# Optimization experiments

Hardware: AMD Instinct MI355X
Metric: run time of the kernel (lower is better)

Reference implementation:

```python
import jax, jax.numpy as jnp
import numpy as np

N, D, C, T = 8192, 64, 100, 30  # samples, embedding_dim, n_classes, n_transforms (initialize_radial_flow n_transforms=30)
LOG_EV_CLAMP = 10.0             # EvidenceScaler clamp on log evidence
EV_BUDGET = 0.5 * D * float(np.log(4.0 * np.pi))  # 'normal' evidence budget: 0.5*dim*log(4*pi)


def setup_inputs() -> dict:
    key = jax.random.key(0)
    ks = jax.random.split(key, 8)
    x = jax.random.normal(ks[0], (N, D), dtype=jnp.float32)          # embeddings (base = identity here)
    labels = jax.random.randint(ks[1], (N,), 0, C)                   # int class labels
    freq = jax.random.uniform(ks[2], (C,), dtype=jnp.float32) + 0.1
    freq = freq / freq.sum()                                         # labels_frequency (sums to 1)
    # per-class radial flow params: z0 [C,T,D], alpha' [C,T], beta' [C,T]
    z0 = jax.random.normal(ks[3], (C, T, D), dtype=jnp.float32) * 0.1
    alpha_prime = jax.random.normal(ks[4], (C, T), dtype=jnp.float32) * 0.1
    beta_prime = jax.random.normal(ks[5], (C, T), dtype=jnp.float32) * 0.1
    W = jax.random.normal(ks[6], (D, C), dtype=jnp.float32) / np.sqrt(D)  # CategoricalOutput linear
    b = jnp.zeros((C,), jnp.float32)
    return dict(x=x, labels=labels, labels_frequency=freq, z0=z0,
                alpha_prime=alpha_prime, beta_prime=beta_prime, W=W, b=b)


def _flow_log_prob(x, z0s, aps, bps):
    """Radial normalizing flow log-density (density direction): log N(f(x)) + log|det df/dx|.
    x: [N, D]; z0s: [T, D]; aps, bps: [T]."""
    def step(carry, params):
        z, ld = carry
        z0, ap, bp = params
        alpha = jax.nn.softplus(ap)
        beta = -alpha + jax.nn.softplus(bp)   # beta > -alpha ensures invertibility
        diff = z - z0                          # [N, D]
        r = jnp.linalg.norm(diff, axis=-1)     # [N]
        h = 1.0 / (alpha + r)
        bh = beta * h
        z_new = z + bh[:, None] * diff
        # log|det| = (D-1)*log(1+beta*h) + log(1 + beta*h + beta*h'*r), h' = -h^2
        ld_new = ld + (D - 1) * jnp.log1p(bh) + jnp.log1p(bh * (1.0 - h * r))
        return (z_new, ld_new), None

    init = (x, jnp.zeros(x.shape[0], x.dtype))
    (z, ld), _ = jax.lax.scan(step, init, (z0s, aps, bps))
    base = -0.5 * (D * jnp.log(2.0 * jnp.pi) + jnp.sum(z * z, axis=-1))  # standard normal base
    return base + ld


def reference(x, labels, labels_frequency, z0, alpha_prime, beta_prime, W, b):
    # per-class flow log-probs for ALL samples: [C, N] (dispatch-compute, vectorized over classes)
    lp = jax.vmap(_flow_log_prob, in_axes=(None, 0, 0, 0))(x, z0, alpha_prime, beta_prime)
    # class_specific_log_prob: gather each sample's own-class log-prob (the boolean-mask gather/scatter loop)
    class_lp = jnp.take_along_axis(lp, labels[None, :], axis=0)[0]            # [N]
    # marginalize_log_prob: logsumexp over classes with log class frequencies
    marg = jax.nn.logsumexp(lp + jnp.log(labels_frequency)[:, None], axis=0)  # [N]
    # EvidenceScaler('normal') + clamp, then NatPN Dirichlet posterior update
    log_ev = jnp.minimum(marg + EV_BUDGET, LOG_EV_CLAMP)                      # [N]
    probs = jax.nn.softmax(x @ W + b, axis=-1)                                # expected sufficient statistics
    alpha = 1.0 + jnp.exp(log_ev)[:, None] * probs                            # prior alpha=1 + evidence*stats
    # output: [N, C+1] = [log alpha | class-specific log-prob]
    return jnp.concatenate([jnp.log(alpha), class_lp[:, None]], axis=1)
```

## Files before the change

### kernel.cpp

```cpp
#include <hip/hip_runtime.h>
#include <math.h>

#define N 8192
#define D 64
#define C 100
#define T 30
#define GSTRIDE 32
#define ZROWS 32
#define CROWS 112
#define WSTRIDE 20
#define SB 16

static constexpr float D_LOG_2PI      = 117.62413225019811f;
static constexpr float EV_BUDGET_F    = 80.992775903017304f;
static constexpr float LOG_EV_CLAMP_F = 10.0f;

typedef __attribute__((ext_vector_type(8))) short short8x;
typedef __attribute__((ext_vector_type(4))) float floatx4;

static __device__ __forceinline__ unsigned short f2bf(float f) {
    __bf16 h = (__bf16)f;
    return __builtin_bit_cast(unsigned short, h);
}

#define AS_CONST __attribute__((address_space(4)))
typedef const AS_CONST floatx4* cfp4_t;
static __device__ __forceinline__ floatx4 sload4(const float* p) {
    return *(cfp4_t)(unsigned long long)p;
}

__global__ __launch_bounds__(256) void megaprep_kernel(
        const float* __restrict__ x,
        const float* __restrict__ z0,
        const float* __restrict__ ap,
        const float* __restrict__ bp,
        const float* __restrict__ W,
        unsigned short* __restrict__ xbf,
        float* __restrict__ q0,
        float* __restrict__ Gp,
        float* __restrict__ abgt,
        unsigned short* __restrict__ z0bf,
        unsigned short* __restrict__ wtbf) {
    const int blk = blockIdx.x;

    if (blk < 256) {
        const int r = blk * 32 + (threadIdx.x >> 3);
        const int e = threadIdx.x & 7;
        const float4* xp = (const float4*)(x + (size_t)r * D + e * 8);
        const float4 a = xp[0], b = xp[1];
        short8x o;
        o[0] = f2bf(a.x); o[1] = f2bf(a.y); o[2] = f2bf(a.z); o[3] = f2bf(a.w);
        o[4] = f2bf(b.x); o[5] = f2bf(b.y); o[6] = f2bf(b.z); o[7] = f2bf(b.w);
        *(short8x*)(xbf + (size_t)r * D + e * 8) = o;
        float q = a.x*a.x + a.y*a.y + a.z*a.z + a.w*a.w
                + b.x*b.x + b.y*b.y + b.z*b.z + b.w*b.w;
        q += __shfl_xor(q, 4, 8);
        q += __shfl_xor(q, 2, 8);
        q += __shfl_xor(q, 1, 8);
        if (e == 0) q0[r] = q;
        return;
    }

    if (blk >= 356) {
        const int i = (blk - 356) * 256 + threadIdx.x;
        const int c = i >> 6, d = i & 63;
        wtbf[i] = f2bf(c < C ? W[d * C + c] : 0.0f);
        return;
    }

    const int c = blk - 256;
    __shared__ float z0s[T * D];
    for (int i = threadIdx.x; i < T * D; i += blockDim.x)
        z0s[i] = z0[c * T * D + i];
    __syncthreads();

    for (int idx = threadIdx.x; idx < T * GSTRIDE; idx += blockDim.x) {
        const int u = idx >> 5, v = idx & 31;
        float s = 0.0f;
        if (v < T) {
            #pragma unroll
            for (int d = 0; d < D; ++d)
                s = fmaf(z0s[u * D + d], z0s[v * D + d], s);
        }
        Gp[(size_t)c * T * GSTRIDE + idx] = s;
    }

    for (int i = threadIdx.x; i < ZROWS * D; i += blockDim.x) {
        const int u = i >> 6;
        z0bf[(size_t)c * ZROWS * D + i] = f2bf(u < T ? z0s[u * D + (i & 63)] : 0.0f);
    }

    if (threadIdx.x < T) {
        const int t = threadIdx.x;
        const float a = ap[c * T + t];
        const float b = bp[c * T + t];
        const float spa = fmaxf(a, 0.0f) + log1pf(expf(-fabsf(a)));
        const float spb = fmaxf(b, 0.0f) + log1pf(expf(-fabsf(b)));
        float gtt = 0.0f;
        #pragma unroll
        for (int d = 0; d < D; ++d)
            gtt = fmaf(z0s[t * D + d], z0s[t * D + d], gtt);
        float* o = abgt + ((size_t)c * T + t) * 4;
        o[0] = spa;
        o[1] = -spa + spb;
        o[2] = gtt;
        o[3] = 0.0f;
    }
}

__global__ __launch_bounds__(256, 2) void flow_kernel(
        const unsigned short* __restrict__ xbf,
        const float* __restrict__ q0g,
        const unsigned short* __restrict__ z0bf,
        const float* __restrict__ Gp,
        const float* __restrict__ abgt,
        float* __restrict__ lp) {
    const int c    = blockIdx.y;
    const int wv   = threadIdx.x >> 6;
    const int ln   = threadIdx.x & 63;
    const int col  = ln & 15;
    const int quad = ln >> 4;
    const int nb   = blockIdx.x * 512 + wv * 128;

    __shared__ float wlds[4][64 * WSTRIDE];

    const unsigned short* zb = z0bf + (size_t)c * ZROWS * D;
    short8x A[2][2];
    #pragma unroll
    for (int mu = 0; mu < 2; ++mu) {
        A[mu][0] = *(const short8x*)(zb + (mu * 16 + col) * D + quad * 8);
        A[mu][1] = *(const short8x*)(zb + (mu * 16 + col) * D + 32 + quad * 8);
    }

    float w[2][ZROWS];
    #pragma unroll
    for (int half = 0; half < 2; ++half) {
        const int hb = nb + half * 64;
        #pragma unroll
        for (int mu = 0; mu < 2; ++mu) {
            floatx4 acc[4];
            #pragma unroll
            for (int nt = 0; nt < 4; ++nt) acc[nt] = (floatx4)(0.0f);
            #pragma unroll
            for (int nt = 0; nt < 4; ++nt) {
                const unsigned short* bp_ =
                    xbf + (size_t)(hb + nt * 16 + col) * D + quad * 8;
                const short8x B0 = *(const short8x*)(bp_);
                acc[nt] = __builtin_amdgcn_mfma_f32_16x16x32_bf16(A[mu][0], B0, acc[nt], 0, 0, 0);
                const short8x B1 = *(const short8x*)(bp_ + 32);
                acc[nt] = __builtin_amdgcn_mfma_f32_16x16x32_bf16(A[mu][1], B1, acc[nt], 0, 0, 0);
            }
            #pragma unroll
            for (int nt = 0; nt < 4; ++nt)
                *(floatx4*)&wlds[wv][(nt * 16 + col) * WSTRIDE + quad * 4] = acc[nt];
            #pragma unroll
            for (int j = 0; j < 4; ++j) {
                const float4 t = *(const float4*)&wlds[wv][ln * WSTRIDE + j * 4];
                w[half][mu * 16 + 4 * j + 0] = t.x;
                w[half][mu * 16 + 4 * j + 1] = t.y;
                w[half][mu * 16 + 4 * j + 2] = t.z;
                w[half][mu * 16 + 4 * j + 3] = t.w;
            }
        }
    }

    const float* gb = Gp + (size_t)c * T * GSTRIDE;
    const float* ab = abgt + ((size_t)c * T) * 4;

    float qA = q0g[nb + ln], qB = q0g[nb + 64 + ln];
    float PA = 1.0f, PB = 1.0f;
    float pfA = 1.0f, pfB = 1.0f;
    float pgA = 1.0f, pgB = 1.0f;
    #pragma unroll
    for (int t = 0; t < T; ++t) {
        const floatx4 av = sload4(ab + t * 4);
        const float alpha = av[0], beta = av[1], Gtt = av[2];

        const float wtA = PA * w[0][t];
        float r2A = fmaf(-2.0f, wtA, qA) + Gtt;
        r2A = fmaxf(r2A, 0.0f);
        const float rA  = __builtin_amdgcn_sqrtf(r2A);
        const float hA  = __builtin_amdgcn_rcpf(alpha + rA);
        const float bhA = beta * hA;
        const float fA  = 1.0f + bhA;
        pfA *= fA;
        pgA *= fmaf(bhA * alpha, hA, 1.0f);
        float qnA = fA * fA * qA;
        qnA = fmaf(bhA * fA, -2.0f * wtA, qnA);
        qnA = fmaf(bhA * bhA, Gtt, qnA);
        qA = qnA;
        const float PnA = PA * fA;
        const float kA  = bhA * __builtin_amdgcn_rcpf(PnA);
        PA = PnA;

        const float wtB = PB * w[1][t];
        float r2B = fmaf(-2.0f, wtB, qB) + Gtt;
        r2B = fmaxf(r2B, 0.0f);
        const float rB  = __builtin_amdgcn_sqrtf(r2B);
        const float hB  = __builtin_amdgcn_rcpf(alpha + rB);
        const float bhB = beta * hB;
        const float fB  = 1.0f + bhB;
        pfB *= fB;
        pgB *= fmaf(bhB * alpha, hB, 1.0f);
        float qnB = fB * fB * qB;
        qnB = fmaf(bhB * fB, -2.0f * wtB, qnB);
        qnB = fmaf(bhB * bhB, Gtt, qnB);
        qB = qnB;
        const float PnB = PB * fB;
        const float kB  = bhB * __builtin_amdgcn_rcpf(PnB);
        PB = PnB;

        #pragma unroll
        for (int m4 = 0; m4 < 8; ++m4) {
            if (m4 < (t >> 2)) continue;
            const floatx4 g = sload4(gb + t * GSTRIDE + 4 * m4);
            w[0][4 * m4 + 0] = fmaf(-kA, g[0], w[0][4 * m4 + 0]);
            w[0][4 * m4 + 1] = fmaf(-kA, g[1], w[0][4 * m4 + 1]);
            w[0][4 * m4 + 2] = fmaf(-kA, g[2], w[0][4 * m4 + 2]);
            w[0][4 * m4 + 3] = fmaf(-kA, g[3], w[0][4 * m4 + 3]);
            w[1][4 * m4 + 0] = fmaf(-kB, g[0], w[1][4 * m4 + 0]);
            w[1][4 * m4 + 1] = fmaf(-kB, g[1], w[1][4 * m4 + 1]);
            w[1][4 * m4 + 2] = fmaf(-kB, g[2], w[1][4 * m4 + 2]);
            w[1][4 * m4 + 3] = fmaf(-kB, g[3], w[1][4 * m4 + 3]);
        }
    }
    const float ldA = 63.0f * __logf(pfA) + __logf(pgA);
    const float ldB = 63.0f * __logf(pfB) + __logf(pgB);

    lp[(size_t)c * N + nb + ln]      = -0.5f * (D_LOG_2PI + qA) + ldA;
    lp[(size_t)c * N + nb + 64 + ln] = -0.5f * (D_LOG_2PI + qB) + ldB;
}

__global__ __launch_bounds__(256) void epilogue_kernel(
        const float* __restrict__ lp,
        const unsigned short* __restrict__ xbf,
        const unsigned short* __restrict__ wtbf,
        const float* __restrict__ b,
        const int* __restrict__ labels,
        const float* __restrict__ freq,
        float* __restrict__ out) {
    const int n0  = blockIdx.x * SB;
    const int tid = threadIdx.x;
    const int wv  = tid >> 6;
    const int ln  = tid & 63;

    __shared__ float lps[SB][101];
    __shared__ float lgs[SB][CROWS];
    __shared__ float lf[C];
    __shared__ float bsm[C];
    __shared__ int   lbl[SB];

    if (wv == 0) {
        const int col  = ln & 15;
        const int quad = ln >> 4;
        const unsigned short* bp_ = xbf + (size_t)(n0 + col) * D + quad * 8;
        const short8x B0 = *(const short8x*)(bp_);
        const short8x B1 = *(const short8x*)(bp_ + 32);
        #pragma unroll
        for (int ct = 0; ct < 7; ++ct) {
            const unsigned short* apq = wtbf + (size_t)(ct * 16 + col) * D + quad * 8;
            const short8x A0 = *(const short8x*)(apq);
            const short8x A1 = *(const short8x*)(apq + 32);
            floatx4 acc = (floatx4)(0.0f);
            acc = __builtin_amdgcn_mfma_f32_16x16x32_bf16(A0, B0, acc, 0, 0, 0);
            acc = __builtin_amdgcn_mfma_f32_16x16x32_bf16(A1, B1, acc, 0, 0, 0);
            #pragma unroll
            for (int j = 0; j < 4; ++j)
                lgs[col][ct * 16 + quad * 4 + j] = acc[j];
        }
    } else {
        for (int i = tid - 64; i < C * SB; i += 192) {
            const int cc = i >> 4, s = i & (SB - 1);
            lps[s][cc] = lp[(size_t)cc * N + n0 + s];
        }
        if (tid - 64 < C) {
            const int t2 = tid - 64;
            lf[t2]  = __logf(freq[t2]);
            bsm[t2] = b[t2];
        }
        if (tid >= 192 && tid < 192 + SB)
            lbl[tid - 192] = labels[n0 + (tid - 192)];
    }
    __syncthreads();

    const int s = tid >> 4;
    const int k = tid & 15;
    const int n = n0 + s;

    float lgt[7];
    float lm = -INFINITY;
    float vm = -INFINITY, vs = 0.0f;
    #pragma unroll
    for (int j = 0; j < 7; ++j) {
        const int cc = k + 16 * j;
        if (cc < C) {
            const float v = lps[s][cc] + lf[cc];
            const float m2 = fmaxf(vm, v);
            vs = vs * __expf(vm - m2) + __expf(v - m2);
            vm = m2;
            lgt[j] = lgs[s][cc] + bsm[cc];
            lm = fmaxf(lm, lgt[j]);
        } else lgt[j] = -INFINITY;
    }

    #pragma unroll
    for (int off = 8; off >= 1; off >>= 1) {
        const float om = __shfl_xor(vm, off, 16);
        const float os = __shfl_xor(vs, off, 16);
        const float m2 = fmaxf(vm, om);
        vs = vs * __expf(vm - m2) + os * __expf(om - m2);
        vm = m2;
        lm = fmaxf(lm, __shfl_xor(lm, off, 16));
    }
    const float marg = vm + __logf(vs);
    const float ev = __expf(fminf(marg + EV_BUDGET_F, LOG_EV_CLAMP_F));

    float ls = 0.0f;
    #pragma unroll
    for (int j = 0; j < 7; ++j)
        if (k + 16 * j < C) ls += __expf(lgt[j] - lm);
    #pragma unroll
    for (int off = 8; off >= 1; off >>= 1)
        ls += __shfl_xor(ls, off, 16);

    const float inv = ev / ls;
    float* __restrict__ outr = out + (size_t)n * (C + 1);
    #pragma unroll
    for (int j = 0; j < 7; ++j) {
        const int cc = k + 16 * j;
        if (cc < C) outr[cc] = log1pf(__expf(lgt[j] - lm) * inv);
    }
    if (k == 0) outr[C] = lps[s][lbl[s]];
}

extern "C" void kernel_launch(void* const* d_in, const int* in_sizes, int n_in,
                              void* d_out, int out_size, void* d_ws, size_t ws_size,
                              hipStream_t stream) {
    const float* x      = (const float*)d_in[0];
    const int*   labels = (const int*)  d_in[1];
    const float* freq   = (const float*)d_in[2];
    const float* z0     = (const float*)d_in[3];
    const float* ap     = (const float*)d_in[4];
    const float* bp     = (const float*)d_in[5];
    const float* W      = (const float*)d_in[6];
    const float* b      = (const float*)d_in[7];
    float* out = (float*)d_out;

    float* ws     = (float*)d_ws;
    float* lp     = ws;
    float* Gp     = lp + (size_t)C * N;
    float* abgt   = Gp + (size_t)C * T * GSTRIDE;
    unsigned short* z0bf = (unsigned short*)(abgt + (size_t)C * T * 4);
    unsigned short* xbf  = z0bf + (size_t)C * ZROWS * D;
    unsigned short* wtbf = xbf + (size_t)N * D;
    float* q0     = (float*)(wtbf + (size_t)CROWS * D);

    megaprep_kernel<<<384, 256, 0, stream>>>(x, z0, ap, bp, W,
                                             xbf, q0, Gp, abgt, z0bf, wtbf);
    flow_kernel<<<dim3(N / 512, C), 256, 0, stream>>>(xbf, q0, z0bf, Gp, abgt, lp);
    epilogue_kernel<<<N / SB, 256, 0, stream>>>(lp, xbf, wtbf, b, labels, freq, out);
}
```

Baseline: 141.5 us.

## Pack flow recurrence into float2 ops with single-wave blocks and cache prefetch

Rewrites the per-sample flow recurrence so the two samples each lane owns are kept in float2 vectors, letting the compiler emit packed FMA/mul instructions (v_pk_fma_f32) for the w updates and q recurrences. The flow kernel is relaunched as 64-thread single-wave blocks over 128 samples each, with a smaller LDS buffer. Each wave also touches the per-class G and alpha/beta tables up front to warm the cache. Packed math roughly halves VALU issue for the dominant update loop, at the cost of more blocks and extra prefetch loads.

Measured after the change: 153.2 us. 1.08x slower.

```diff
diff --git a/kernel.cpp b/kernel.cpp
--- a/kernel.cpp
+++ b/kernel.cpp
@@ -17,6 +17,7 @@
 
 typedef __attribute__((ext_vector_type(8))) short short8x;
 typedef __attribute__((ext_vector_type(4))) float floatx4;
+typedef __attribute__((ext_vector_type(2))) float floatx2;
 
 static __device__ __forceinline__ unsigned short f2bf(float f) {
     __bf16 h = (__bf16)f;
@@ -27,6 +28,13 @@
 typedef const AS_CONST floatx4* cfp4_t;
 static __device__ __forceinline__ floatx4 sload4(const float* p) {
     return *(cfp4_t)(unsigned long long)p;
+}
+
+static __device__ __forceinline__ floatx2 sp(float s) {
+    floatx2 v; v.x = s; v.y = s; return v;
+}
+static __device__ __forceinline__ floatx2 fma2(floatx2 a, floatx2 b, floatx2 c) {
+    return __builtin_elementwise_fma(a, b, c);
 }
 
 __global__ __launch_bounds__(256) void megaprep_kernel(
@@ -108,7 +116,7 @@
     }
 }
 
-__global__ __launch_bounds__(256, 2) void flow_kernel(
+__global__ __launch_bounds__(64, 4) void flow_kernel(
         const unsigned short* __restrict__ xbf,
         const float* __restrict__ q0g,
         const unsigned short* __restrict__ z0bf,
@@ -116,13 +124,26 @@
         const float* __restrict__ abgt,
         float* __restrict__ lp) {
     const int c    = blockIdx.y;
-    const int wv   = threadIdx.x >> 6;
-    const int ln   = threadIdx.x & 63;
+    const int ln   = threadIdx.x;
     const int col  = ln & 15;
     const int quad = ln >> 4;
-    const int nb   = blockIdx.x * 512 + wv * 128;
-
-    __shared__ float wlds[4][64 * WSTRIDE];
+    const int nb   = blockIdx.x * 128;
+
+    __shared__ float wlds[64 * WSTRIDE];
+
+    const float* gb = Gp + (size_t)c * T * GSTRIDE;
+    const float* ab = abgt + ((size_t)c * T) * 4;
+
+    {
+        const float4* gpre = (const float4*)gb;
+        const float4 d0 = gpre[ln];
+        const float4 d1 = gpre[ln + 64];
+        const float4 d2 = gpre[ln + 128];
+        const float4 d3 = gpre[ln + 176];
+        const float4* apre = (const float4*)ab;
+        const float4 d4 = apre[ln < 30 ? ln : 29];
+        asm volatile("" :: "v"(d0.x), "v"(d1.x), "v"(d2.x), "v"(d3.x), "v"(d4.x));
+    }
 
     const unsigned short* zb = z0bf + (size_t)c * ZROWS * D;
     short8x A[2][2];
@@ -132,7 +153,7 @@
         A[mu][1] = *(const short8x*)(zb + (mu * 16 + col) * D + 32 + quad * 8);
     }
 
-    float w[2][ZROWS];
+    floatx2 w2[ZROWS];
     #pragma unroll
     for (int half = 0; half < 2; ++half) {
         const int hb = nb + half * 64;
@@ -152,83 +173,78 @@
             }
             #pragma unroll
             for (int nt = 0; nt < 4; ++nt)
-                *(floatx4*)&wlds[wv][(nt * 16 + col) * WSTRIDE + quad * 4] = acc[nt];
+                *(floatx4*)&wlds[(nt * 16 + col) * WSTRIDE + quad * 4] = acc[nt];
             #pragma unroll
             for (int j = 0; j < 4; ++j) {
-                const float4 t = *(const float4*)&wlds[wv][ln * WSTRIDE + j * 4];
-                w[half][mu * 16 + 4 * j + 0] = t.x;
-                w[half][mu * 16 + 4 * j + 1] = t.y;
-                w[half][mu * 16 + 4 * j + 2] = t.z;
-                w[half][mu * 16 + 4 * j + 3] = t.w;
+                const float4 t = *(const float4*)&wlds[ln * WSTRIDE + j * 4];
+                if (half == 0) {
+                    w2[mu * 16 + 4 * j + 0].x = t.x;
+                    w2[mu * 16 + 4 * j + 1].x = t.y;
+                    w2[mu * 16 + 4 * j + 2].x = t.z;
+                    w2[mu * 16 + 4 * j + 3].x = t.w;
+                } else {
+                    w2[mu * 16 + 4 * j + 0].y = t.x;
+                    w2[mu * 16 + 4 * j + 1].y = t.y;
+                    w2[mu * 16 + 4 * j + 2].y = t.z;
+                    w2[mu * 16 + 4 * j + 3].y = t.w;
+                }
             }
         }
     }
 
-    const float* gb = Gp + (size_t)c * T * GSTRIDE;
-    const float* ab = abgt + ((size_t)c * T) * 4;
-
-    float qA = q0g[nb + ln], qB = q0g[nb + 64 + ln];
-    float PA = 1.0f, PB = 1.0f;
-    float pfA = 1.0f, pfB = 1.0f;
-    float pgA = 1.0f, pgB = 1.0f;
+    floatx2 q2;
+    q2.x = q0g[nb + ln];
+    q2.y = q0g[nb + 64 + ln];
+    floatx2 P2  = sp(1.0f);
+    floatx2 pf2 = sp(1.0f);
+    floatx2 pg2 = sp(1.0f);
     #pragma unroll
     for (int t = 0; t < T; ++t) {
         const floatx4 av = sload4(ab + t * 4);
         const float alpha = av[0], beta = av[1], Gtt = av[2];
 
-        const float wtA = PA * w[0][t];
-        float r2A = fmaf(-2.0f, wtA, qA) + Gtt;
-        r2A = fmaxf(r2A, 0.0f);
-        const float rA  = __builtin_amdgcn_sqrtf(r2A);
-        const float hA  = __builtin_amdgcn_rcpf(alpha + rA);
-        const float bhA = beta * hA;
-        const float fA  = 1.0f + bhA;
-        pfA *= fA;
-        pgA *= fmaf(bhA * alpha, hA, 1.0f);
-        float qnA = fA * fA * qA;
-        qnA = fmaf(bhA * fA, -2.0f * wtA, qnA);
-        qnA = fmaf(bhA * bhA, Gtt, qnA);
-        qA = qnA;
-        const float PnA = PA * fA;
-        const float kA  = bhA * __builtin_amdgcn_rcpf(PnA);
-        PA = PnA;
-
-        const float wtB = PB * w[1][t];
-        float r2B = fmaf(-2.0f, wtB, qB) + Gtt;
-        r2B = fmaxf(r2B, 0.0f);
-        const float rB  = __builtin_amdgcn_sqrtf(r2B);
-        const float hB  = __builtin_amdgcn_rcpf(alpha + rB);
-        const float bhB = beta * hB;
-        const float fB  = 1.0f + bhB;
-        pfB *= fB;
-        pgB *= fmaf(bhB * alpha, hB, 1.0f);
-        float qnB = fB * fB * qB;
-        qnB = fmaf(bhB * fB, -2.0f * wtB, qnB);
-        qnB = fmaf(bhB * bhB, Gtt, qnB);
-        qB = qnB;
-        const float PnB = PB * fB;
-        const float kB  = bhB * __builtin_amdgcn_rcpf(PnB);
-        PB = PnB;
+        const floatx2 wt2 = P2 * w2[t];
+        const floatx2 nw2 = sp(-2.0f) * wt2;
+        floatx2 r2v = (q2 + nw2) + sp(Gtt);
+        r2v.x = fmaxf(r2v.x, 0.0f);
+        r2v.y = fmaxf(r2v.y, 0.0f);
+        floatx2 r_;
+        r_.x = __builtin_amdgcn_sqrtf(r2v.x);
+        r_.y = __builtin_amdgcn_sqrtf(r2v.y);
+        const floatx2 ar = r_ + sp(alpha);
+        floatx2 h2;
+        h2.x = __builtin_amdgcn_rcpf(ar.x);
+        h2.y = __builtin_amdgcn_rcpf(ar.y);
+        const floatx2 bh2 = sp(beta) * h2;
+        const floatx2 f2v = sp(1.0f) + bh2;
+        pf2 *= f2v;
+        pg2 *= fma2(bh2 * sp(alpha), h2, sp(1.0f));
+        floatx2 qn2 = (f2v * f2v) * q2;
+        qn2 = fma2(bh2 * f2v, nw2, qn2);
+        qn2 = fma2(bh2 * bh2, sp(Gtt), qn2);
+        q2 = qn2;
+        const floatx2 Pn2 = P2 * f2v;
+        floatx2 ip2;
+        ip2.x = __builtin_amdgcn_rcpf(Pn2.x);
+        ip2.y = __builtin_amdgcn_rcpf(Pn2.y);
+        const floatx2 nk2 = -(bh2 * ip2);
+        P2 = Pn2;
 
         #pragma unroll
         for (int m4 = 0; m4 < 8; ++m4) {
             if (m4 < (t >> 2)) continue;
             const floatx4 g = sload4(gb + t * GSTRIDE + 4 * m4);
-            w[0][4 * m4 + 0] = fmaf(-kA, g[0], w[0][4 * m4 + 0]);
-            w[0][4 * m4 + 1] = fmaf(-kA, g[1], w[0][4 * m4 + 1]);
-            w[0][4 * m4 + 2] = fmaf(-kA, g[2], w[0][4 * m4 + 2]);
-            w[0][4 * m4 + 3] = fmaf(-kA, g[3], w[0][4 * m4 + 3]);
-            w[1][4 * m4 + 0] = fmaf(-kB, g[0], w[1][4 * m4 + 0]);
-            w[1][4 * m4 + 1] = fmaf(-kB, g[1], w[1][4 * m4 + 1]);
-            w[1][4 * m4 + 2] = fmaf(-kB, g[2], w[1][4 * m4 + 2]);
-            w[1][4 * m4 + 3] = fmaf(-kB, g[3], w[1][4 * m4 + 3]);
-        }
-    }
-    const float ldA = 63.0f * __logf(pfA) + __logf(pgA);
-    const float ldB = 63.0f * __logf(pfB) + __logf(pgB);
-
-    lp[(size_t)c * N + nb + ln]      = -0.5f * (D_LOG_2PI + qA) + ldA;
-    lp[(size_t)c * N + nb + 64 + ln] = -0.5f * (D_LOG_2PI + qB) + ldB;
+            w2[4 * m4 + 0] = fma2(nk2, sp(g[0]), w2[4 * m4 + 0]);
+            w2[4 * m4 + 1] = fma2(nk2, sp(g[1]), w2[4 * m4 + 1]);
+            w2[4 * m4 + 2] = fma2(nk2, sp(g[2]), w2[4 * m4 + 2]);
+            w2[4 * m4 + 3] = fma2(nk2, sp(g[3]), w2[4 * m4 + 3]);
+        }
+    }
+    const float ldA = 63.0f * __logf(pf2.x) + __logf(pg2.x);
+    const float ldB = 63.0f * __logf(pf2.y) + __logf(pg2.y);
+
+    lp[(size_t)c * N + nb + ln]      = -0.5f * (D_LOG_2PI + q2.x) + ldA;
+    lp[(size_t)c * N + nb + 64 + ln] = -0.5f * (D_LOG_2PI + q2.y) + ldB;
 }
 
 __global__ __launch_bounds__(256) void epilogue_kernel(
@@ -357,6 +373,6 @@
 
     megaprep_kernel<<<384, 256, 0, stream>>>(x, z0, ap, bp, W,
                                              xbf, q0, Gp, abgt, z0bf, wtbf);
-    flow_kernel<<<dim3(N / 512, C), 256, 0, stream>>>(xbf, q0, z0bf, Gp, abgt, lp);
+    flow_kernel<<<dim3(N / 128, C), 64, 0, stream>>>(xbf, q0, z0bf, Gp, abgt, lp);
     epilogue_kernel<<<N / SB, 256, 0, stream>>>(lp, xbf, wtbf, b, labels, freq, out);
 }
```

## Process four sample groups per lane in flow kernel and prefetch flow params

Applied to the files above, without the earlier changes.

Each thread now carries four 64-sample groups through the 30-step radial flow recurrence instead of two, which halves the grid along N. The per-step scalar parameter loads and G-matrix loads are amortized over twice as many samples, and the four independent chains expose more instruction-level parallelism. A dummy prefetch of the per-class G and alpha/beta tables is added at kernel start to warm the cache. The change roughly doubles register pressure for the w arrays (4x32 floats) under launch_bounds(256,2), which risks spills or lower occupancy, and gives fewer blocks (800 vs 1600) to fill the GPU.

Result: faster. 135.0 us (-4.5%).

```diff
diff --git a/kernel.cpp b/kernel.cpp
--- a/kernel.cpp
+++ b/kernel.cpp
@@ -120,9 +120,22 @@
     const int ln   = threadIdx.x & 63;
     const int col  = ln & 15;
     const int quad = ln >> 4;
-    const int nb   = blockIdx.x * 512 + wv * 128;
+    const int nb   = blockIdx.x * 1024 + wv * 256;
 
     __shared__ float wlds[4][64 * WSTRIDE];
+
+    const float* gb = Gp + (size_t)c * T * GSTRIDE;
+    const float* ab = abgt + ((size_t)c * T) * 4;
+
+    {
+        const float4* gpre = (const float4*)gb;
+        const int gi = threadIdx.x < 240 ? threadIdx.x : 239;
+        const float4 d0 = gpre[gi];
+        const float4* apre = (const float4*)ab;
+        const int ai = (threadIdx.x & 31) < 30 ? (threadIdx.x & 31) : 29;
+        const float4 d1 = apre[ai];
+        asm volatile("" :: "v"(d0.x), "v"(d1.x));
+    }
 
     const unsigned short* zb = z0bf + (size_t)c * ZROWS * D;
     short8x A[2][2];
@@ -132,9 +145,9 @@
         A[mu][1] = *(const short8x*)(zb + (mu * 16 + col) * D + 32 + quad * 8);
     }
 
-    float w[2][ZROWS];
-    #pragma unroll
-    for (int half = 0; half < 2; ++half) {
+    float w[4][ZROWS];
+    #pragma unroll
+    for (int half = 0; half < 4; ++half) {
         const int hb = nb + half * 64;
         #pragma unroll
         for (int mu = 0; mu < 2; ++mu) {
@@ -164,71 +177,60 @@
         }
     }
 
-    const float* gb = Gp + (size_t)c * T * GSTRIDE;
-    const float* ab = abgt + ((size_t)c * T) * 4;
-
-    float qA = q0g[nb + ln], qB = q0g[nb + 64 + ln];
-    float PA = 1.0f, PB = 1.0f;
-    float pfA = 1.0f, pfB = 1.0f;
-    float pgA = 1.0f, pgB = 1.0f;
+    float q[4], P[4], pf[4], pg[4];
+    #pragma unroll
+    for (int s = 0; s < 4; ++s) {
+        q[s]  = q0g[nb + s * 64 + ln];
+        P[s]  = 1.0f;
+        pf[s] = 1.0f;
+        pg[s] = 1.0f;
+    }
+
     #pragma unroll
     for (int t = 0; t < T; ++t) {
         const floatx4 av = sload4(ab + t * 4);
         const float alpha = av[0], beta = av[1], Gtt = av[2];
 
-        const float wtA = PA * w[0][t];
-        float r2A = fmaf(-2.0f, wtA, qA) + Gtt;
-        r2A = fmaxf(r2A, 0.0f);
-        const float rA  = __builtin_amdgcn_sqrtf(r2A);
-        const float hA  = __builtin_amdgcn_rcpf(alpha + rA);
-        const float bhA = beta * hA;
-        const float fA  = 1.0f + bhA;
-        pfA *= fA;
-        pgA *= fmaf(bhA * alpha, hA, 1.0f);
-        float qnA = fA * fA * qA;
-        qnA = fmaf(bhA * fA, -2.0f * wtA, qnA);
-        qnA = fmaf(bhA * bhA, Gtt, qnA);
-        qA = qnA;
-        const float PnA = PA * fA;
-        const float kA  = bhA * __builtin_amdgcn_rcpf(PnA);
-        PA = PnA;
-
-        const float wtB = PB * w[1][t];
-        float r2B = fmaf(-2.0f, wtB, qB) + Gtt;
-        r2B = fmaxf(r2B, 0.0f);
-        const float rB  = __builtin_amdgcn_sqrtf(r2B);
-        const float hB  = __builtin_amdgcn_rcpf(alpha + rB);
-        const float bhB = beta * hB;
-        const float fB  = 1.0f + bhB;
-        pfB *= fB;
-        pgB *= fmaf(bhB * alpha, hB, 1.0f);
-        float qnB = fB * fB * qB;
-        qnB = fmaf(bhB * fB, -2.0f * wtB, qnB);
-        qnB = fmaf(bhB * bhB, Gtt, qnB);
-        qB = qnB;
-        const float PnB = PB * fB;
-        const float kB  = bhB * __builtin_amdgcn_rcpf(PnB);
-        PB = PnB;
+        float nk[4];
+        #pragma unroll
+        for (int s = 0; s < 4; ++s) {
+            const float wt = P[s] * w[s][t];
+            float r2 = fmaf(-2.0f, wt, q[s]) + Gtt;
+            r2 = fmaxf(r2, 0.0f);
+            const float r  = __builtin_amdgcn_sqrtf(r2);
+            const float h  = __builtin_amdgcn_rcpf(alpha + r);
+            const float bh = beta * h;
+            const float f  = 1.0f + bh;
+            pf[s] *= f;
+            pg[s] *= fmaf(bh * alpha, h, 1.0f);
+            float qn = f * f * q[s];
+            qn = fmaf(bh * f, -2.0f * wt, qn);
+            qn = fmaf(bh * bh, Gtt, qn);
+            q[s] = qn;
+            const float Pn = P[s] * f;
+            nk[s] = -(bh * __builtin_amdgcn_rcpf(Pn));
+            P[s] = Pn;
+        }
 
         #pragma unroll
         for (int m4 = 0; m4 < 8; ++m4) {
             if (m4 < (t >> 2)) continue;
             const floatx4 g = sload4(gb + t * GSTRIDE + 4 * m4);
-            w[0][4 * m4 + 0] = fmaf(-kA, g[0], w[0][4 * m4 + 0]);
-            w[0][4 * m4 + 1] = fmaf(-kA, g[1], w[0][4 * m4 + 1]);
-            w[0][4 * m4 + 2] = fmaf(-kA, g[2], w[0][4 * m4 + 2]);
-            w[0][4 * m4 + 3] = fmaf(-kA, g[3], w[0][4 * m4 + 3]);
-            w[1][4 * m4 + 0] = fmaf(-kB, g[0], w[1][4 * m4 + 0]);
-            w[1][4 * m4 + 1] = fmaf(-kB, g[1], w[1][4 * m4 + 1]);
-            w[1][4 * m4 + 2] = fmaf(-kB, g[2], w[1][4 * m4 + 2]);
-            w[1][4 * m4 + 3] = fmaf(-kB, g[3], w[1][4 * m4 + 3]);
-        }
-    }
-    const float ldA = 63.0f * __logf(pfA) + __logf(pgA);
-    const float ldB = 63.0f * __logf(pfB) + __logf(pgB);
-
-    lp[(size_t)c * N + nb + ln]      = -0.5f * (D_LOG_2PI + qA) + ldA;
-    lp[(size_t)c * N + nb + 64 + ln] = -0.5f * (D_LOG_2PI + qB) + ldB;
+            #pragma unroll
+            for (int s = 0; s < 4; ++s) {
+                w[s][4 * m4 + 0] = fmaf(nk[s], g[0], w[s][4 * m4 + 0]);
+                w[s][4 * m4 + 1] = fmaf(nk[s], g[1], w[s][4 * m4 + 1]);
+                w[s][4 * m4 + 2] = fmaf(nk[s], g[2], w[s][4 * m4 + 2]);
+                w[s][4 * m4 + 3] = fmaf(nk[s], g[3], w[s][4 * m4 + 3]);
+            }
+        }
+    }
+
+    #pragma unroll
+    for (int s = 0; s < 4; ++s) {
+        const float ld = 63.0f * __logf(pf[s]) + __logf(pg[s]);
+        lp[(size_t)c * N + nb + s * 64 + ln] = -0.5f * (D_LOG_2PI + q[s]) + ld;
+    }
 }
 
 __global__ __launch_bounds__(256) void epilogue_kernel(
@@ -357,6 +359,6 @@
 
     megaprep_kernel<<<384, 256, 0, stream>>>(x, z0, ap, bp, W,
                                              xbf, q0, Gp, abgt, z0bf, wtbf);
-    flow_kernel<<<dim3(N / 512, C), 256, 0, stream>>>(xbf, q0, z0bf, Gp, abgt, lp);
+    flow_kernel<<<dim3(N / 1024, C), 256, 0, stream>>>(xbf, q0, z0bf, Gp, abgt, lp);
     epilogue_kernel<<<N / SB, 256, 0, stream>>>(lp, xbf, wtbf, b, labels, freq, out);
 }
```
